# Performance work log

Measured on AMD Instinct MI355X. Metric: run time of the kernel, lower is better.

The kernel has to match this reference:

```python
import jax, jax.numpy as jnp
import numpy as np

TOP_K = 2


def setup_inputs() -> dict:
    key = jax.random.key(0)
    ks = jax.random.split(key, 5)
    B, S, D, F, E = 2, 2048, 1024, 3584, 8
    scale_in = 1.0 / np.sqrt(D)
    scale_f = 1.0 / np.sqrt(F)
    return {
        "hidden_states": jax.random.normal(ks[0], (B, S, D), dtype=jnp.float32),
        "gate_w": jax.random.normal(ks[1], (E, D), dtype=jnp.float32) * scale_in,
        "w1": jax.random.normal(ks[2], (E, F, D), dtype=jnp.float32) * scale_in,
        "w3": jax.random.normal(ks[3], (E, F, D), dtype=jnp.float32) * scale_in,
        "w2": jax.random.normal(ks[4], (E, D, F), dtype=jnp.float32) * scale_f,
    }


def _routing_weights(logits):
    # softmax over experts, select top-k, renormalize (Mixtral semantics)
    probs = jax.nn.softmax(logits, axis=-1)          # [T, E]
    topv, topi = jax.lax.top_k(probs, TOP_K)          # [T, k]
    topv = topv / jnp.sum(topv, axis=-1, keepdims=True)
    T, E = logits.shape
    w = jnp.zeros((T, E), dtype=logits.dtype)
    w = w.at[jnp.arange(T)[:, None], topi].set(topv)  # dense [T, E] routing weights
    return w


def reference(hidden_states, gate_w, w1, w3, w2):
    B, S, D = hidden_states.shape
    x = hidden_states.reshape(-1, D)                  # [T, D]
    logits = x @ gate_w.T                             # [T, E]
    rw = _routing_weights(logits)                     # [T, E]
    E = gate_w.shape[0]
    out = jnp.zeros_like(x)
    for e in range(E):                                # fixed small expert count
        h = jax.nn.silu(x @ w1[e].T) * (x @ w3[e].T)  # [T, F]
        out = out + rw[:, e:e + 1] * (h @ w2[e].T)    # [T, D]
    return out.reshape(B, S, D)
```

## Files before the change

### kernel.cpp

```cpp
#include <hip/hip_runtime.h>
#include <hip/hip_bf16.h>


#define T_TOK 4096
#define DIM   1024
#define FF    3584
#define NE    8
#define BM    128
#define CAP   (T_TOK*2 + NE*BM)

using f32x4 = __attribute__((ext_vector_type(4))) float;
using s16x8 = __attribute__((ext_vector_type(8))) short;

__device__ __forceinline__ ushort f2b(float f) {
    __hip_bfloat16 b = __float2bfloat16(f);
    ushort u; __builtin_memcpy(&u, &b, 2); return u;
}

__global__ __launch_bounds__(256)
void k_route(const float* __restrict__ x, const float* __restrict__ gw,
             int* __restrict__ topi, float* __restrict__ topw, int* __restrict__ counts)
{
    __shared__ float gws[NE*DIM];
    const int tid = threadIdx.x;
    for (int i = tid; i < NE*DIM/4; i += 256)
        ((float4*)gws)[i] = ((const float4*)gw)[i];
    __syncthreads();

    const int lane = tid & 63, wid = tid >> 6;
    const int t = blockIdx.x*4 + wid;

    float4 xr[4];
    const float4* xrow = (const float4*)(x + (size_t)t*DIM) + lane*4;
    #pragma unroll
    for (int i = 0; i < 4; ++i) xr[i] = xrow[i];

    float lg[NE];
    #pragma unroll
    for (int e = 0; e < NE; ++e) {
        const float4* g4 = (const float4*)(gws + e*DIM) + lane*4;
        float s = 0.f;
        #pragma unroll
        for (int i = 0; i < 4; ++i) {
            float4 g = g4[i];
            s += xr[i].x*g.x + xr[i].y*g.y + xr[i].z*g.z + xr[i].w*g.w;
        }
        #pragma unroll
        for (int off = 32; off; off >>= 1) s += __shfl_xor(s, off);
        lg[e] = s;
    }
    if (lane == 0) {
        float b1 = -1e30f, b2 = -1e30f; int i1 = 0, i2 = 0;
        #pragma unroll
        for (int e = 0; e < NE; ++e) {
            float v = lg[e];
            if (v > b1)      { b2 = b1; i2 = i1; b1 = v; i1 = e; }
            else if (v > b2) { b2 = v; i2 = e; }
        }
        float p2 = __expf(b2 - b1);
        float inv = 1.f / (1.f + p2);
        topi[2*t]   = i1; topi[2*t+1] = i2;
        topw[2*t]   = inv; topw[2*t+1] = p2*inv;
        atomicAdd(&counts[i1], 1); atomicAdd(&counts[i2], 1);
    }
}

__global__ void k_scan(const int* __restrict__ counts, int* __restrict__ offs,
                       int* __restrict__ rowTok)
{
    if (threadIdx.x == 0) {
        int acc = 0; offs[0] = 0;
        for (int e = 0; e < NE; ++e) {
            int p = (counts[e] + BM - 1) & ~(BM - 1);
            acc += p; offs[e+1] = acc;
        }
    }
    for (int i = threadIdx.x; i < CAP; i += blockDim.x) rowTok[i] = -1;
}

__global__ __launch_bounds__(256)
void k_scatter(const int* __restrict__ topi, const float* __restrict__ topw,
               const int* __restrict__ offs, int* __restrict__ cursor,
               int* __restrict__ rowTok, float* __restrict__ rowW)
{
    int t = blockIdx.x*256 + threadIdx.x;
    #pragma unroll
    for (int j = 0; j < 2; ++j) {
        int e = topi[2*t + j];
        int pos = offs[e] + atomicAdd(&cursor[e], 1);
        rowTok[pos] = t;
        rowW[pos] = topw[2*t + j];
    }
}

__global__ __launch_bounds__(256)
void k_cvt(const float* __restrict__ x, ushort* __restrict__ xb)
{
    size_t i = (size_t)blockIdx.x*256 + threadIdx.x;
    const float4* src = (const float4*)x + i*2;
    float4 v0 = src[0], v1 = src[1];
    uint4 o;
    o.x = f2b(v0.x) | ((uint)f2b(v0.y) << 16);
    o.y = f2b(v0.z) | ((uint)f2b(v0.w) << 16);
    o.z = f2b(v1.x) | ((uint)f2b(v1.y) << 16);
    o.w = f2b(v1.z) | ((uint)f2b(v1.w) << 16);
    ((uint4*)xb)[i] = o;
}

__global__ __launch_bounds__(256, 2)
void k_gemm1(const ushort* __restrict__ xb,
             const float* __restrict__ w1g, const float* __restrict__ w3g,
             const int* __restrict__ offs, const int* __restrict__ rowTok,
             ushort* __restrict__ hout)
{
    __shared__ __align__(16) ushort As[2][128*64];
    __shared__ __align__(16) ushort Bs[2][128*64];
    const int rowStart = blockIdx.y * BM;
    if (rowStart >= offs[8]) return;
    int e = 0;
    #pragma unroll
    for (int k = 1; k < NE; ++k) if (rowStart >= offs[k]) e = k;

    const int fc = blockIdx.x * 64;
    const float* __restrict__ W1 = w1g + ((size_t)e*FF + fc)*DIM;
    const float* __restrict__ W3 = w3g + ((size_t)e*FF + fc)*DIM;

    const int tid = threadIdx.x;
    const int lane = tid & 63, wid = tid >> 6;
    const int wr = wid >> 1, wc = wid & 1;
    const int lo = lane & 15, hi = lane >> 4;

    const int aRowB = tid >> 3;
    const int aC8   = tid & 7;
    const int bRowB = tid >> 4;
    const int bC4   = tid & 15;

    int atok[4];
    #pragma unroll
    for (int p = 0; p < 4; ++p) atok[p] = rowTok[rowStart + p*32 + aRowB];

    uint4  ar[4];
    float4 br[8];

    auto loadT = [&](int kt) {
        const int k0 = kt * 64;
        #pragma unroll
        for (int p = 0; p < 4; ++p) {
            if (atok[p] >= 0)
                ar[p] = *(const uint4*)(xb + (size_t)atok[p]*DIM + k0 + aC8*8);
            else
                ar[p] = uint4{0u,0u,0u,0u};
        }
        #pragma unroll
        for (int p = 0; p < 8; ++p) {
            int r = p*16 + bRowB;
            const float* src = (p < 4) ? (W1 + (size_t)r*DIM) : (W3 + (size_t)(r-64)*DIM);
            br[p] = *(const float4*)(src + k0 + bC4*4);
        }
    };
    auto storeT = [&](int buf) {
        char* Ab = (char*)As[buf];
        #pragma unroll
        for (int p = 0; p < 4; ++p) {
            int r = p*32 + aRowB;
            *(uint4*)(Ab + r*128 + ((aC8*16) ^ ((r&7)<<4))) = ar[p];
        }
        char* Bb = (char*)Bs[buf];
        #pragma unroll
        for (int p = 0; p < 8; ++p) {
            int r = p*16 + bRowB;
            ushort4 c;
            c.x = f2b(br[p].x); c.y = f2b(br[p].y);
            c.z = f2b(br[p].z); c.w = f2b(br[p].w);
            *(ushort4*)(Bb + r*128 + ((bC4*8) ^ ((r&7)<<4))) = c;
        }
    };

    f32x4 acc1[4][2], acc3[4][2];
    #pragma unroll
    for (int m = 0; m < 4; ++m)
        #pragma unroll
        for (int n = 0; n < 2; ++n) { acc1[m][n] = (f32x4)(0.f); acc3[m][n] = (f32x4)(0.f); }

    auto compute = [&](int buf) {
        char* Ab = (char*)As[buf];
        char* Bb = (char*)Bs[buf];
        #pragma unroll
        for (int kk = 0; kk < 2; ++kk) {
            s16x8 a[4], b1[2], b3[2];
            #pragma unroll
            for (int m = 0; m < 4; ++m) {
                int r = wr*64 + m*16 + lo;
                a[m] = *(const s16x8*)(Ab + r*128 + ((kk*64 + hi*16) ^ ((r&7)<<4)));
            }
            #pragma unroll
            for (int n = 0; n < 2; ++n) {
                int r1 = wc*32 + n*16 + lo;
                b1[n] = *(const s16x8*)(Bb + r1*128 + ((kk*64 + hi*16) ^ ((r1&7)<<4)));
                int r3 = r1 + 64;
                b3[n] = *(const s16x8*)(Bb + r3*128 + ((kk*64 + hi*16) ^ ((r3&7)<<4)));
            }
            #pragma unroll
            for (int m = 0; m < 4; ++m)
                #pragma unroll
                for (int n = 0; n < 2; ++n) {
                    acc1[m][n] = __builtin_amdgcn_mfma_f32_16x16x32_bf16(a[m], b1[n], acc1[m][n], 0, 0, 0);
                    acc3[m][n] = __builtin_amdgcn_mfma_f32_16x16x32_bf16(a[m], b3[n], acc3[m][n], 0, 0, 0);
                }
        }
    };

    loadT(0); storeT(0); __syncthreads();
    int cur = 0;
    const int NK = DIM/64;
    for (int kt = 0; kt < NK; ++kt) {
        bool more = (kt + 1 < NK);
        if (more) loadT(kt + 1);
        compute(cur);
        if (more) storeT(cur ^ 1);
        __syncthreads();
        cur ^= 1;
    }

    #pragma unroll
    for (int m = 0; m < 4; ++m)
        #pragma unroll
        for (int n = 0; n < 2; ++n) {
            f32x4 v1 = acc1[m][n], v3 = acc3[m][n];
            int col = fc + wc*32 + n*16 + lo;
            #pragma unroll
            for (int j = 0; j < 4; ++j) {
                int row = wr*64 + m*16 + hi*4 + j;
                float s = v1[j];
                float val = (s / (1.f + __expf(-s))) * v3[j];
                hout[(size_t)(rowStart + row)*FF + col] = f2b(val);
            }
        }
}

__global__ __launch_bounds__(256, 2)
void k_gemm2(const ushort* __restrict__ h,
             const float* __restrict__ w2g,
             const int* __restrict__ offs, const int* __restrict__ rowTok,
             const float* __restrict__ rowW, float* __restrict__ out)
{
    __shared__ __align__(16) ushort As[2][128*64];
    __shared__ __align__(16) ushort Bs[2][128*64];
    const int rowStart = blockIdx.y * BM;
    if (rowStart >= offs[8]) return;
    int e = 0;
    #pragma unroll
    for (int k = 1; k < NE; ++k) if (rowStart >= offs[k]) e = k;

    const int dc = blockIdx.x * 128;
    const float* __restrict__ W2 = w2g + ((size_t)e*DIM + dc)*FF;

    const int tid = threadIdx.x;
    const int lane = tid & 63, wid = tid >> 6;
    const int wr = wid >> 1, wc = wid & 1;
    const int lo = lane & 15, hi = lane >> 4;

    const int aRowB = tid >> 3;
    const int aC8   = tid & 7;
    const int bRowB = tid >> 4;
    const int bC4   = tid & 15;

    uint4  ar[4];
    float4 br[8];

    auto loadT = [&](int kt) {
        const int k0 = kt * 64;
        #pragma unroll
        for (int p = 0; p < 4; ++p) {
            int r = p*32 + aRowB;
            ar[p] = *(const uint4*)(h + (size_t)(rowStart + r)*FF + k0 + aC8*8);
        }
        #pragma unroll
        for (int p = 0; p < 8; ++p) {
            int r = p*16 + bRowB;
            br[p] = *(const float4*)(W2 + (size_t)r*FF + k0 + bC4*4);
        }
    };
    auto storeT = [&](int buf) {
        char* Ab = (char*)As[buf];
        #pragma unroll
        for (int p = 0; p < 4; ++p) {
            int r = p*32 + aRowB;
            *(uint4*)(Ab + r*128 + ((aC8*16) ^ ((r&7)<<4))) = ar[p];
        }
        char* Bb = (char*)Bs[buf];
        #pragma unroll
        for (int p = 0; p < 8; ++p) {
            int r = p*16 + bRowB;
            ushort4 c;
            c.x = f2b(br[p].x); c.y = f2b(br[p].y);
            c.z = f2b(br[p].z); c.w = f2b(br[p].w);
            *(ushort4*)(Bb + r*128 + ((bC4*8) ^ ((r&7)<<4))) = c;
        }
    };

    f32x4 acc[4][4];
    #pragma unroll
    for (int m = 0; m < 4; ++m)
        #pragma unroll
        for (int n = 0; n < 4; ++n) acc[m][n] = (f32x4)(0.f);

    auto compute = [&](int buf) {
        char* Ab = (char*)As[buf];
        char* Bb = (char*)Bs[buf];
        #pragma unroll
        for (int kk = 0; kk < 2; ++kk) {
            s16x8 a[4], b[4];
            #pragma unroll
            for (int m = 0; m < 4; ++m) {
                int r = wr*64 + m*16 + lo;
                a[m] = *(const s16x8*)(Ab + r*128 + ((kk*64 + hi*16) ^ ((r&7)<<4)));
            }
            #pragma unroll
            for (int n = 0; n < 4; ++n) {
                int r = wc*64 + n*16 + lo;
                b[n] = *(const s16x8*)(Bb + r*128 + ((kk*64 + hi*16) ^ ((r&7)<<4)));
            }
            #pragma unroll
            for (int m = 0; m < 4; ++m)
                #pragma unroll
                for (int n = 0; n < 4; ++n)
                    acc[m][n] = __builtin_amdgcn_mfma_f32_16x16x32_bf16(a[m], b[n], acc[m][n], 0, 0, 0);
        }
    };

    loadT(0); storeT(0); __syncthreads();
    int cur = 0;
    const int NK = FF/64;
    for (int kt = 0; kt < NK; ++kt) {
        bool more = (kt + 1 < NK);
        if (more) loadT(kt + 1);
        compute(cur);
        if (more) storeT(cur ^ 1);
        __syncthreads();
        cur ^= 1;
    }

    #pragma unroll
    for (int m = 0; m < 4; ++m)
        #pragma unroll
        for (int j = 0; j < 4; ++j) {
            int prow = rowStart + wr*64 + m*16 + hi*4 + j;
            int tok = rowTok[prow];
            if (tok < 0) continue;
            float w = rowW[prow];
            #pragma unroll
            for (int n = 0; n < 4; ++n) {
                int d = dc + wc*64 + n*16 + lo;
                atomicAdd(&out[(size_t)tok*DIM + d], w * acc[m][n][j]);
            }
        }
}

extern "C" void kernel_launch(void* const* d_in, const int* in_sizes, int n_in,
                              void* d_out, int out_size, void* d_ws, size_t ws_size,
                              hipStream_t stream)
{
    const float* x  = (const float*)d_in[0];
    const float* gw = (const float*)d_in[1];
    const float* w1 = (const float*)d_in[2];
    const float* w3 = (const float*)d_in[3];
    const float* w2 = (const float*)d_in[4];
    float* out = (float*)d_out;
    char* ws = (char*)d_ws;

    int*    counts = (int*)ws;
    int*    cursor = counts + 8;
    int*    offs   = counts + 16;
    int*    topi   = (int*)  (ws + 256);
    float*  topw   = (float*)(ws + 256 + (size_t)T_TOK*8);
    int*    rowTok = (int*)  (ws + 256 + (size_t)T_TOK*16);
    float*  rowW   = (float*)(ws + 256 + (size_t)T_TOK*16 + (size_t)CAP*4);
    ushort* xb     = (ushort*)(ws + 139520);
    ushort* h      = (ushort*)(ws + 8528128);

    hipMemsetAsync(ws, 0, 256, stream);
    hipMemsetAsync(d_out, 0, (size_t)T_TOK*DIM*4, stream);

    k_route  <<<T_TOK/4, 256, 0, stream>>>(x, gw, topi, topw, counts);
    k_scan   <<<1, 256, 0, stream>>>(counts, offs, rowTok);
    k_scatter<<<T_TOK/256, 256, 0, stream>>>(topi, topw, offs, cursor, rowTok, rowW);
    k_cvt    <<<(T_TOK*DIM/8)/256, 256, 0, stream>>>(x, xb);
    k_gemm1  <<<dim3(FF/64,  CAP/BM), 256, 0, stream>>>(xb, w1, w3, offs, rowTok, h);
    k_gemm2  <<<dim3(DIM/128, CAP/BM), 256, 0, stream>>>(h, w2, offs, rowTok, rowW, out);
}
```

Measured before the change: 519.3 us.

## Pre-convert expert weights to bf16, stage tiles via global_load_lds, replace atomics with combine

Adds conversion kernels that write w1/w3 (interleaved per 64-row chunk) and w2 to bf16 in the workspace. Both GEMMs then stage A and B tiles straight into LDS with global_load_lds, which drops the register round trip and the in-loop fp32-to-bf16 conversion. The LDS layout loses its XOR swizzle, so bank conflicts may rise. GEMM2 now writes per-row bf16 results instead of doing atomicAdd on the fp32 output, and a new combine kernel gathers each token's two expert rows and applies the routing weights. The cost is a full weight conversion pass on every call, extra workspace traffic, and bf16 rounding of the expert outputs before they are combined.

```diff
diff --git a/kernel.cpp b/kernel.cpp
--- a/kernel.cpp
+++ b/kernel.cpp
@@ -9,12 +9,40 @@
 #define BM    128
 #define CAP   (T_TOK*2 + NE*BM)
 
+#define OFF_TOPI   256UL
+#define OFF_TOPW   33024UL
+#define OFF_TOKPOS 65792UL
+#define OFF_ROWTOK 98560UL
+#define OFF_XB     135424UL
+#define OFF_BIG    8524032UL
+#define OFF_W2B    OFF_BIG
+#define OFF_RES    (OFF_BIG + 58720256UL)
+#define OFF_H      (OFF_BIG + 117440512UL)
+#define WS_NEED    (OFF_H + 66060288UL)
+
 using f32x4 = __attribute__((ext_vector_type(4))) float;
 using s16x8 = __attribute__((ext_vector_type(8))) short;
 
 __device__ __forceinline__ ushort f2b(float f) {
     __hip_bfloat16 b = __float2bfloat16(f);
     ushort u; __builtin_memcpy(&u, &b, 2); return u;
+}
+__device__ __forceinline__ float blo(uint u){ u <<= 16; float f; __builtin_memcpy(&f,&u,4); return f; }
+__device__ __forceinline__ float bhi(uint u){ u &= 0xFFFF0000u; float f; __builtin_memcpy(&f,&u,4); return f; }
+
+__device__ __forceinline__ void gl_lds16(const ushort* g, ushort* l) {
+    __builtin_amdgcn_global_load_lds(
+        (const __attribute__((address_space(1))) void*)g,
+        (__attribute__((address_space(3))) void*)l, 16, 0, 0);
+}
+
+__device__ __forceinline__ uint4 pack8(float4 v0, float4 v1) {
+    uint4 o;
+    o.x = f2b(v0.x) | ((uint)f2b(v0.y) << 16);
+    o.y = f2b(v0.z) | ((uint)f2b(v0.w) << 16);
+    o.z = f2b(v1.x) | ((uint)f2b(v1.y) << 16);
+    o.w = f2b(v1.z) | ((uint)f2b(v1.w) << 16);
+    return o;
 }
 
 __global__ __launch_bounds__(256)
@@ -79,9 +107,9 @@
 }
 
 __global__ __launch_bounds__(256)
-void k_scatter(const int* __restrict__ topi, const float* __restrict__ topw,
+void k_scatter(const int* __restrict__ topi,
                const int* __restrict__ offs, int* __restrict__ cursor,
-               int* __restrict__ rowTok, float* __restrict__ rowW)
+               int* __restrict__ rowTok, int* __restrict__ tokPos)
 {
     int t = blockIdx.x*256 + threadIdx.x;
     #pragma unroll
@@ -89,27 +117,38 @@
         int e = topi[2*t + j];
         int pos = offs[e] + atomicAdd(&cursor[e], 1);
         rowTok[pos] = t;
-        rowW[pos] = topw[2*t + j];
-    }
-}
-
-__global__ __launch_bounds__(256)
-void k_cvt(const float* __restrict__ x, ushort* __restrict__ xb)
+        tokPos[2*t + j] = pos;
+    }
+}
+
+__global__ __launch_bounds__(256)
+void k_cvt(const float* __restrict__ src, ushort* __restrict__ dst)
 {
     size_t i = (size_t)blockIdx.x*256 + threadIdx.x;
-    const float4* src = (const float4*)x + i*2;
-    float4 v0 = src[0], v1 = src[1];
-    uint4 o;
-    o.x = f2b(v0.x) | ((uint)f2b(v0.y) << 16);
-    o.y = f2b(v0.z) | ((uint)f2b(v0.w) << 16);
-    o.z = f2b(v1.x) | ((uint)f2b(v1.y) << 16);
-    o.w = f2b(v1.z) | ((uint)f2b(v1.w) << 16);
-    ((uint4*)xb)[i] = o;
+    float4 v0 = ((const float4*)src)[2*i], v1 = ((const float4*)src)[2*i+1];
+    ((uint4*)dst)[i] = pack8(v0, v1);
+}
+
+__global__ __launch_bounds__(256)
+void k_cvt13(const float* __restrict__ w1, const float* __restrict__ w3,
+             ushort* __restrict__ w13)
+{
+    int i = blockIdx.x*256 + threadIdx.x;
+    int k8 = i & 127;
+    int rd = i >> 7;
+    int e   = rd / 7168;
+    int rem = rd - e*7168;
+    int c   = rem >> 7;
+    int rem2= rem & 127;
+    int s   = rem2 >> 6;
+    int r   = rem2 & 63;
+    const float* src = (s ? w3 : w1) + ((size_t)e*FF + c*64 + r)*DIM + k8*8;
+    float4 v0 = ((const float4*)src)[0], v1 = ((const float4*)src)[1];
+    ((uint4*)w13)[i] = pack8(v0, v1);
 }
 
 __global__ __launch_bounds__(256, 2)
-void k_gemm1(const ushort* __restrict__ xb,
-             const float* __restrict__ w1g, const float* __restrict__ w3g,
+void k_gemm1(const ushort* __restrict__ xb, const ushort* __restrict__ w13,
              const int* __restrict__ offs, const int* __restrict__ rowTok,
              ushort* __restrict__ hout)
 {
@@ -121,60 +160,35 @@
     #pragma unroll
     for (int k = 1; k < NE; ++k) if (rowStart >= offs[k]) e = k;
 
-    const int fc = blockIdx.x * 64;
-    const float* __restrict__ W1 = w1g + ((size_t)e*FF + fc)*DIM;
-    const float* __restrict__ W3 = w3g + ((size_t)e*FF + fc)*DIM;
+    const int fc2 = blockIdx.x;
+    const ushort* Wb = w13 + ((size_t)(e*56 + fc2) * 128) * DIM;
 
     const int tid = threadIdx.x;
     const int lane = tid & 63, wid = tid >> 6;
     const int wr = wid >> 1, wc = wid & 1;
     const int lo = lane & 15, hi = lane >> 4;
-
-    const int aRowB = tid >> 3;
-    const int aC8   = tid & 7;
-    const int bRowB = tid >> 4;
-    const int bC4   = tid & 15;
-
-    int atok[4];
-    #pragma unroll
-    for (int p = 0; p < 4; ++p) atok[p] = rowTok[rowStart + p*32 + aRowB];
-
-    uint4  ar[4];
-    float4 br[8];
-
-    auto loadT = [&](int kt) {
-        const int k0 = kt * 64;
-        #pragma unroll
-        for (int p = 0; p < 4; ++p) {
-            if (atok[p] >= 0)
-                ar[p] = *(const uint4*)(xb + (size_t)atok[p]*DIM + k0 + aC8*8);
-            else
-                ar[p] = uint4{0u,0u,0u,0u};
-        }
-        #pragma unroll
-        for (int p = 0; p < 8; ++p) {
-            int r = p*16 + bRowB;
-            const float* src = (p < 4) ? (W1 + (size_t)r*DIM) : (W3 + (size_t)(r-64)*DIM);
-            br[p] = *(const float4*)(src + k0 + bC4*4);
+    const int lr = lane >> 3;
+    const int lc = lane & 7;
+
+    const ushort* aSrc[4];
+    const ushort* bSrc[4];
+    #pragma unroll
+    for (int i = 0; i < 4; ++i) {
+        int row = wid*32 + i*8 + lr;
+        int tok = rowTok[rowStart + row]; if (tok < 0) tok = 0;
+        aSrc[i] = xb + (size_t)tok*DIM + lc*8;
+        bSrc[i] = Wb + (size_t)row*DIM + lc*8;
+    }
+
+    auto stage = [&](int buf, int kt) {
+        ushort* Ab = &As[buf][0] + wid*4*512;
+        ushort* Bb = &Bs[buf][0] + wid*4*512;
+        #pragma unroll
+        for (int i = 0; i < 4; ++i) {
+            gl_lds16(aSrc[i] + kt*64, Ab + i*512);
+            gl_lds16(bSrc[i] + kt*64, Bb + i*512);
         }
     };
-    auto storeT = [&](int buf) {
-        char* Ab = (char*)As[buf];
-        #pragma unroll
-        for (int p = 0; p < 4; ++p) {
-            int r = p*32 + aRowB;
-            *(uint4*)(Ab + r*128 + ((aC8*16) ^ ((r&7)<<4))) = ar[p];
-        }
-        char* Bb = (char*)Bs[buf];
-        #pragma unroll
-        for (int p = 0; p < 8; ++p) {
-            int r = p*16 + bRowB;
-            ushort4 c;
-            c.x = f2b(br[p].x); c.y = f2b(br[p].y);
-            c.z = f2b(br[p].z); c.w = f2b(br[p].w);
-            *(ushort4*)(Bb + r*128 + ((bC4*8) ^ ((r&7)<<4))) = c;
-        }
-    };
 
     f32x4 acc1[4][2], acc3[4][2];
     #pragma unroll
@@ -183,22 +197,18 @@
         for (int n = 0; n < 2; ++n) { acc1[m][n] = (f32x4)(0.f); acc3[m][n] = (f32x4)(0.f); }
 
     auto compute = [&](int buf) {
-        char* Ab = (char*)As[buf];
-        char* Bb = (char*)Bs[buf];
+        const ushort* Ab = &As[buf][0];
+        const ushort* Bb = &Bs[buf][0];
         #pragma unroll
         for (int kk = 0; kk < 2; ++kk) {
             s16x8 a[4], b1[2], b3[2];
             #pragma unroll
-            for (int m = 0; m < 4; ++m) {
-                int r = wr*64 + m*16 + lo;
-                a[m] = *(const s16x8*)(Ab + r*128 + ((kk*64 + hi*16) ^ ((r&7)<<4)));
-            }
+            for (int m = 0; m < 4; ++m)
+                a[m] = *(const s16x8*)(Ab + (wr*64 + m*16 + lo)*64 + kk*32 + hi*8);
             #pragma unroll
             for (int n = 0; n < 2; ++n) {
-                int r1 = wc*32 + n*16 + lo;
-                b1[n] = *(const s16x8*)(Bb + r1*128 + ((kk*64 + hi*16) ^ ((r1&7)<<4)));
-                int r3 = r1 + 64;
-                b3[n] = *(const s16x8*)(Bb + r3*128 + ((kk*64 + hi*16) ^ ((r3&7)<<4)));
+                b1[n] = *(const s16x8*)(Bb + (wc*32 + n*16 + lo)*64 + kk*32 + hi*8);
+                b3[n] = *(const s16x8*)(Bb + (64 + wc*32 + n*16 + lo)*64 + kk*32 + hi*8);
             }
             #pragma unroll
             for (int m = 0; m < 4; ++m)
@@ -210,18 +220,18 @@
         }
     };
 
-    loadT(0); storeT(0); __syncthreads();
+    stage(0, 0);
+    __syncthreads();
     int cur = 0;
     const int NK = DIM/64;
     for (int kt = 0; kt < NK; ++kt) {
-        bool more = (kt + 1 < NK);
-        if (more) loadT(kt + 1);
+        if (kt + 1 < NK) stage(cur ^ 1, kt + 1);
         compute(cur);
-        if (more) storeT(cur ^ 1);
         __syncthreads();
         cur ^= 1;
     }
 
+    const int fc = fc2 * 64;
     #pragma unroll
     for (int m = 0; m < 4; ++m)
         #pragma unroll
@@ -239,10 +249,8 @@
 }
 
 __global__ __launch_bounds__(256, 2)
-void k_gemm2(const ushort* __restrict__ h,
-             const float* __restrict__ w2g,
-             const int* __restrict__ offs, const int* __restrict__ rowTok,
-             const float* __restrict__ rowW, float* __restrict__ out)
+void k_gemm2(const ushort* __restrict__ h, const ushort* __restrict__ w2b,
+             const int* __restrict__ offs, ushort* __restrict__ res)
 {
     __shared__ __align__(16) ushort As[2][128*64];
     __shared__ __align__(16) ushort Bs[2][128*64];
@@ -253,51 +261,33 @@
     for (int k = 1; k < NE; ++k) if (rowStart >= offs[k]) e = k;
 
     const int dc = blockIdx.x * 128;
-    const float* __restrict__ W2 = w2g + ((size_t)e*DIM + dc)*FF;
+    const ushort* Wb = w2b + ((size_t)e*DIM + dc)*FF;
 
     const int tid = threadIdx.x;
     const int lane = tid & 63, wid = tid >> 6;
     const int wr = wid >> 1, wc = wid & 1;
     const int lo = lane & 15, hi = lane >> 4;
-
-    const int aRowB = tid >> 3;
-    const int aC8   = tid & 7;
-    const int bRowB = tid >> 4;
-    const int bC4   = tid & 15;
-
-    uint4  ar[4];
-    float4 br[8];
-
-    auto loadT = [&](int kt) {
-        const int k0 = kt * 64;
-        #pragma unroll
-        for (int p = 0; p < 4; ++p) {
-            int r = p*32 + aRowB;
-            ar[p] = *(const uint4*)(h + (size_t)(rowStart + r)*FF + k0 + aC8*8);
-        }
-        #pragma unroll
-        for (int p = 0; p < 8; ++p) {
-            int r = p*16 + bRowB;
-            br[p] = *(const float4*)(W2 + (size_t)r*FF + k0 + bC4*4);
+    const int lr = lane >> 3;
+    const int lc = lane & 7;
+
+    const ushort* aSrc[4];
+    const ushort* bSrc[4];
+    #pragma unroll
+    for (int i = 0; i < 4; ++i) {
+        int row = wid*32 + i*8 + lr;
+        aSrc[i] = h  + (size_t)(rowStart + row)*FF + lc*8;
+        bSrc[i] = Wb + (size_t)row*FF + lc*8;
+    }
+
+    auto stage = [&](int buf, int kt) {
+        ushort* Ab = &As[buf][0] + wid*4*512;
+        ushort* Bb = &Bs[buf][0] + wid*4*512;
+        #pragma unroll
+        for (int i = 0; i < 4; ++i) {
+            gl_lds16(aSrc[i] + kt*64, Ab + i*512);
+            gl_lds16(bSrc[i] + kt*64, Bb + i*512);
         }
     };
-    auto storeT = [&](int buf) {
-        char* Ab = (char*)As[buf];
-        #pragma unroll
-        for (int p = 0; p < 4; ++p) {
-            int r = p*32 + aRowB;
-            *(uint4*)(Ab + r*128 + ((aC8*16) ^ ((r&7)<<4))) = ar[p];
-        }
-        char* Bb = (char*)Bs[buf];
-        #pragma unroll
-        for (int p = 0; p < 8; ++p) {
-            int r = p*16 + bRowB;
-            ushort4 c;
-            c.x = f2b(br[p].x); c.y = f2b(br[p].y);
-            c.z = f2b(br[p].z); c.w = f2b(br[p].w);
-            *(ushort4*)(Bb + r*128 + ((bC4*8) ^ ((r&7)<<4))) = c;
-        }
-    };
 
     f32x4 acc[4][4];
     #pragma unroll
@@ -306,21 +296,17 @@
         for (int n = 0; n < 4; ++n) acc[m][n] = (f32x4)(0.f);
 
     auto compute = [&](int buf) {
-        char* Ab = (char*)As[buf];
-        char* Bb = (char*)Bs[buf];
+        const ushort* Ab = &As[buf][0];
+        const ushort* Bb = &Bs[buf][0];
         #pragma unroll
         for (int kk = 0; kk < 2; ++kk) {
             s16x8 a[4], b[4];
             #pragma unroll
-            for (int m = 0; m < 4; ++m) {
-                int r = wr*64 + m*16 + lo;
-                a[m] = *(const s16x8*)(Ab + r*128 + ((kk*64 + hi*16) ^ ((r&7)<<4)));
-            }
-            #pragma unroll
-            for (int n = 0; n < 4; ++n) {
-                int r = wc*64 + n*16 + lo;
-                b[n] = *(const s16x8*)(Bb + r*128 + ((kk*64 + hi*16) ^ ((r&7)<<4)));
-            }
+            for (int m = 0; m < 4; ++m)
+                a[m] = *(const s16x8*)(Ab + (wr*64 + m*16 + lo)*64 + kk*32 + hi*8);
+            #pragma unroll
+            for (int n = 0; n < 4; ++n)
+                b[n] = *(const s16x8*)(Bb + (wc*64 + n*16 + lo)*64 + kk*32 + hi*8);
             #pragma unroll
             for (int m = 0; m < 4; ++m)
                 #pragma unroll
@@ -329,14 +315,13 @@
         }
     };
 
-    loadT(0); storeT(0); __syncthreads();
+    stage(0, 0);
+    __syncthreads();
     int cur = 0;
     const int NK = FF/64;
     for (int kt = 0; kt < NK; ++kt) {
-        bool more = (kt + 1 < NK);
-        if (more) loadT(kt + 1);
+        if (kt + 1 < NK) stage(cur ^ 1, kt + 1);
         compute(cur);
-        if (more) storeT(cur ^ 1);
         __syncthreads();
         cur ^= 1;
     }
@@ -346,15 +331,32 @@
         #pragma unroll
         for (int j = 0; j < 4; ++j) {
             int prow = rowStart + wr*64 + m*16 + hi*4 + j;
-            int tok = rowTok[prow];
-            if (tok < 0) continue;
-            float w = rowW[prow];
             #pragma unroll
             for (int n = 0; n < 4; ++n) {
                 int d = dc + wc*64 + n*16 + lo;
-                atomicAdd(&out[(size_t)tok*DIM + d], w * acc[m][n][j]);
+                res[(size_t)prow*DIM + d] = f2b(acc[m][n][j]);
             }
         }
+}
+
+__global__ __launch_bounds__(256)
+void k_combine(const ushort* __restrict__ res, const int* __restrict__ tokPos,
+               const float* __restrict__ topw, float* __restrict__ out)
+{
+    int i = blockIdx.x*256 + threadIdx.x;
+    int t = i >> 7;
+    int g = i & 127;
+    int pA = tokPos[2*t], pB = tokPos[2*t+1];
+    float wA = topw[2*t], wB = topw[2*t+1];
+    uint4 a = *(const uint4*)(res + (size_t)pA*DIM + g*8);
+    uint4 b = *(const uint4*)(res + (size_t)pB*DIM + g*8);
+    float4 o0, o1;
+    o0.x = wA*blo(a.x) + wB*blo(b.x);  o0.y = wA*bhi(a.x) + wB*bhi(b.x);
+    o0.z = wA*blo(a.y) + wB*blo(b.y);  o0.w = wA*bhi(a.y) + wB*bhi(b.y);
+    o1.x = wA*blo(a.z) + wB*blo(b.z);  o1.y = wA*bhi(a.z) + wB*bhi(b.z);
+    o1.z = wA*blo(a.w) + wB*blo(b.w);  o1.w = wA*bhi(a.w) + wB*bhi(b.w);
+    float4* dst = (float4*)(out + (size_t)t*DIM + g*8);
+    dst[0] = o0; dst[1] = o1;
 }
 
 extern "C" void kernel_launch(void* const* d_in, const int* in_sizes, int n_in,
@@ -368,24 +370,30 @@
     const float* w2 = (const float*)d_in[4];
     float* out = (float*)d_out;
     char* ws = (char*)d_ws;
+    if (ws_size < WS_NEED) return;
 
     int*    counts = (int*)ws;
     int*    cursor = counts + 8;
     int*    offs   = counts + 16;
-    int*    topi   = (int*)  (ws + 256);
-    float*  topw   = (float*)(ws + 256 + (size_t)T_TOK*8);
-    int*    rowTok = (int*)  (ws + 256 + (size_t)T_TOK*16);
-    float*  rowW   = (float*)(ws + 256 + (size_t)T_TOK*16 + (size_t)CAP*4);
-    ushort* xb     = (ushort*)(ws + 139520);
-    ushort* h      = (ushort*)(ws + 8528128);
+    int*    topi   = (int*)  (ws + OFF_TOPI);
+    float*  topw   = (float*)(ws + OFF_TOPW);
+    int*    tokPos = (int*)  (ws + OFF_TOKPOS);
+    int*    rowTok = (int*)  (ws + OFF_ROWTOK);
+    ushort* xb     = (ushort*)(ws + OFF_XB);
+    ushort* w13b   = (ushort*)(ws + OFF_BIG);
+    ushort* w2b    = (ushort*)(ws + OFF_W2B);
+    ushort* res    = (ushort*)(ws + OFF_RES);
+    ushort* h      = (ushort*)(ws + OFF_H);
 
     hipMemsetAsync(ws, 0, 256, stream);
-    hipMemsetAsync(d_out, 0, (size_t)T_TOK*DIM*4, stream);
 
     k_route  <<<T_TOK/4, 256, 0, stream>>>(x, gw, topi, topw, counts);
     k_scan   <<<1, 256, 0, stream>>>(counts, offs, rowTok);
-    k_scatter<<<T_TOK/256, 256, 0, stream>>>(topi, topw, offs, cursor, rowTok, rowW);
+    k_scatter<<<T_TOK/256, 256, 0, stream>>>(topi, offs, cursor, rowTok, tokPos);
     k_cvt    <<<(T_TOK*DIM/8)/256, 256, 0, stream>>>(x, xb);
-    k_gemm1  <<<dim3(FF/64,  CAP/BM), 256, 0, stream>>>(xb, w1, w3, offs, rowTok, h);
-    k_gemm2  <<<dim3(DIM/128, CAP/BM), 256, 0, stream>>>(h, w2, offs, rowTok, rowW, out);
-}
+    k_cvt13  <<<(2*NE*FF*DIM/8)/256, 256, 0, stream>>>(w1, w3, w13b);
+    k_gemm1  <<<dim3(FF/64,  CAP/BM), 256, 0, stream>>>(xb, w13b, offs, rowTok, h);
+    k_cvt    <<<(NE*DIM*FF/8)/256, 256, 0, stream>>>(w2, w2b);
+    k_gemm2  <<<dim3(DIM/128, CAP/BM), 256, 0, stream>>>(h, w2b, offs, res);
+    k_combine<<<(T_TOK*DIM/8)/256, 256, 0, stream>>>(res, tokPos, topw, out);
+}
```

Measured after the change: 696.1 us. 34.0% more time.
